# Optimization experiments

Measured on AMD Instinct MI355X. Metric: run time of the kernel, lower is better.

Reference implementation:

```python
import jax, jax.numpy as jnp
import numpy as np

B, S, D = 32, 1024, 1024   # batch, seq_len, d_model
P, F = 4, 4096             # num_phases, d_ff
# Each phase owns a contiguous split of S/P sequence positions (set_splits builds
# a disjoint contiguous partition of the sequence; assert t == seq_length).


def setup_inputs() -> dict:
    key = jax.random.key(0)
    ks = jax.random.split(key, 6)
    x = jax.random.normal(ks[0], (B, S, D), dtype=jnp.float32)
    phases = jax.random.randint(ks[1], (B, S), 0, P, dtype=jnp.int32)
    s1 = 1.0 / np.sqrt(D)
    s2 = 1.0 / np.sqrt(F)
    W1 = jax.random.uniform(ks[2], (P, D, F), jnp.float32, -s1, s1)
    b1 = jax.random.uniform(ks[3], (P, F), jnp.float32, -s1, s1)
    W2 = jax.random.uniform(ks[4], (P, F, D), jnp.float32, -s2, s2)
    b2 = jax.random.uniform(ks[5], (P, D), jnp.float32, -s2, s2)
    return {"x": x, "W1": W1, "b1": b1, "W2": W2, "b2": b2, "phases": phases}


def reference(x, W1, b1, W2, b2, phases):
    # Branched path (phases.ndim > 1): gather each phase's contiguous split,
    # run that phase's FF, scatter back. Since the static phase_mask is a
    # contiguous equal partition, gather/scatter == reshape into [B, P, S/P, D].
    xs = x.reshape(B, P, S // P, D)
    h = jax.nn.relu(jnp.einsum('bpsd,pdf->bpsf', xs, W1) + b1[None, :, None, :])
    y = jnp.einsum('bpsf,pfd->bpsd', h, W2) + b2[None, :, None, :]
    return y.reshape(B, S, D)
```

## Files before the change

### kernel.cpp

```cpp
#include <hip/hip_runtime.h>
#include <hip/hip_bf16.h>
#include <stdint.h>

typedef __bf16 bf16_t;
typedef bf16_t bf16x8 __attribute__((ext_vector_type(8)));
typedef bf16_t bf16x4 __attribute__((ext_vector_type(4)));
typedef float  f32x4  __attribute__((ext_vector_type(4)));

#define AS1(p) ((const __attribute__((address_space(1))) void*)(p))
#define AS3(p) ((__attribute__((address_space(3))) void*)(p))

static constexpr int B_ = 32, S_ = 1024, D_ = 1024, P_ = 4, F_ = 4096;
static constexpr int SPP = S_ / P_;
static constexpr int MP  = B_ * SPP;

__global__ void conv_x_kernel(const float* __restrict__ x, bf16_t* __restrict__ xg) {
  const int64_t n4 = (int64_t)B_ * S_ * D_ / 4;
  for (int64_t i = (int64_t)blockIdx.x * blockDim.x + threadIdx.x; i < n4;
       i += (int64_t)gridDim.x * blockDim.x) {
    int64_t e = i << 2;
    int d = (int)(e & (D_ - 1));
    int s = (int)((e >> 10) & (S_ - 1));
    int b = (int)(e >> 20);
    int p = s >> 8;
    int r = (b << 8) | (s & 255);
    const float4 v = ((const float4*)x)[i];
    bf16x4 o;
    o[0] = (bf16_t)v.x; o[1] = (bf16_t)v.y; o[2] = (bf16_t)v.z; o[3] = (bf16_t)v.w;
    *(bf16x4*)&xg[(((int64_t)p * MP + r) << 10) | d] = o;
  }
}

__global__ void conv_wt_kernel(const float* __restrict__ W, bf16_t* __restrict__ Wt,
                               int K, int N) {
  __shared__ bf16_t tile[32][33];
  const int p = blockIdx.z;
  const float* Wp = W + (int64_t)p * K * N;
  bf16_t* Wtp = Wt + (int64_t)p * K * N;
  const int n0 = blockIdx.x * 32, k0 = blockIdx.y * 32;
  const int tx = threadIdx.x & 31, ty = threadIdx.x >> 5;
  #pragma unroll
  for (int j = 0; j < 4; ++j) {
    int kr = ty + j * 8;
    tile[kr][tx] = (bf16_t)Wp[(int64_t)(k0 + kr) * N + n0 + tx];
  }
  __syncthreads();
  #pragma unroll
  for (int j = 0; j < 4; ++j) {
    int nr = ty + j * 8;
    Wtp[(int64_t)(n0 + nr) * K + k0 + tx] = tile[tx][nr];
  }
}


__device__ __forceinline__ bf16x8 ldsfrag(const char* region, int row, int cb) {
  return *(const bf16x8*)(region + row * 128 + (cb ^ ((row & 7) << 4)));
}

template<int LDK>
__device__ __forceinline__ void stage_half(const bf16_t* gsrc, char* ldsreg, int t) {
  #pragma unroll
  for (int j = 0; j < 2; ++j) {
    const int idx = j * 512 + t;
    const int row = idx >> 3;
    const int cb  = ((idx & 7) << 4) ^ ((row & 7) << 4);
    __builtin_amdgcn_global_load_lds(AS1((const char*)(gsrc + (int64_t)row * LDK) + cb),
                                     AS3(ldsreg + idx * 16), 16, 0, 0);
  }
}

#define MFMA_QUAD(AF, BF, MO, NO) \
  do { _Pragma("unroll") for (int m_ = 0; m_ < 4; ++m_) \
       _Pragma("unroll") for (int n_ = 0; n_ < 2; ++n_) \
       _Pragma("unroll") for (int k_ = 0; k_ < 2; ++k_) \
         acc[(MO) + m_][(NO) + n_] = __builtin_amdgcn_mfma_f32_16x16x32_bf16( \
             AF[m_][k_], BF[n_][k_], acc[(MO) + m_][(NO) + n_], 0, 0, 0); } while (0)

#define READ_A4(DST, REG, MO) \
  do { _Pragma("unroll") for (int m_ = 0; m_ < 4; ++m_) \
       _Pragma("unroll") for (int k_ = 0; k_ < 2; ++k_) \
         DST[m_][k_] = ldsfrag(REG, wm * 128 + ((MO) + m_) * 16 + fr, k_ * 64 + hi * 16); } while (0)

#define READ_B2(DST, REG, NO) \
  do { _Pragma("unroll") for (int n_ = 0; n_ < 2; ++n_) \
       _Pragma("unroll") for (int k_ = 0; k_ < 2; ++k_) \
         DST[n_][k_] = ldsfrag(REG, wn * 64 + ((NO) + n_) * 16 + fr, k_ * 64 + hi * 16); } while (0)

#define BAR()   __builtin_amdgcn_s_barrier()
#define SBAR()  __builtin_amdgcn_sched_barrier(0)
#define PRIO(x) __builtin_amdgcn_s_setprio(x)
#define VMCNT6() asm volatile("s_waitcnt vmcnt(6)" ::: "memory")
#define VMCNT0() asm volatile("s_waitcnt vmcnt(0)" ::: "memory")

template<bool RELU, bool OUT_BF16, int KK, int NN>
__global__ __launch_bounds__(512, 2)
void ffgemm8_kernel(const bf16_t* __restrict__ A, const bf16_t* __restrict__ Bt,
                    const float* __restrict__ bias, void* __restrict__ outv, int M) {
  static_assert(KK % 128 == 0, "need even number of 64-wide K tiles");
  __shared__ __align__(16) char smem[131072];
  char* const At0 = smem;
  char* const At1 = smem + 32768;
  char* const Bs0 = smem + 65536;
  char* const Bs1 = smem + 98304;

  const int t = threadIdx.x, lane = t & 63, w = t >> 6;
  const int wm = w >> 2, wn = w & 3;
  const int fr = lane & 15, hi = lane >> 4;

  const int gx = gridDim.x, gy = gridDim.y;
  const int nwg = gx * gy * (int)gridDim.z;
  const int id  = ((int)blockIdx.z * gy + (int)blockIdx.y) * gx + (int)blockIdx.x;
  const int swz = (id & 7) * (nwg >> 3) + (id >> 3);
  const int per_p = gx * gy;
  const int p  = swz / per_p;
  const int q  = swz % per_p;
  const int band = q / (gx * 4), qq = q % (gx * 4);
  const int bx = qq >> 2, by = band * 4 + (qq & 3);

  const int tile_m = by * 256, tile_n = bx * 256;
  const bf16_t* Ab = A  + (int64_t)p * M  * KK + (int64_t)tile_m * KK;
  const bf16_t* Bb = Bt + (int64_t)p * NN * KK + (int64_t)tile_n * KK;
  const float* biasp = bias + (int64_t)p * NN;

  f32x4 acc[8][4] = {};
  constexpr int NI = KK / 128;

  stage_half<KK>(Ab,                          At0,          t);
  stage_half<KK>(Ab + (int64_t)128 * KK,      At0 + 16384,  t);
  stage_half<KK>(Bb,                          Bs0,          t);
  stage_half<KK>(Bb + (int64_t)128 * KK,      Bs0 + 16384,  t);
  stage_half<KK>(Bb + 64,                     Bs1,          t);
  stage_half<KK>(Bb + (int64_t)128 * KK + 64, Bs1 + 16384,  t);
  stage_half<KK>(Ab + 64,                     At1,          t);
  VMCNT6();
  BAR(); SBAR();

  for (int i = 0; i < NI; ++i) {
    const int k0 = i * 128;
    const bool more = (i < NI - 1);
    bf16x8 a0[4][2], a1[4][2], b0[2][2], b1[2][2];

    READ_A4(a0, At0, 0); READ_B2(b0, Bs0, 0);
    PRIO(1); MFMA_QUAD(a0, b0, 0, 0); PRIO(0);
    READ_B2(b1, Bs0, 2);
    stage_half<KK>(Ab + (int64_t)128 * KK + (k0 + 64), At1 + 16384, t);
    SBAR(); BAR();
    PRIO(1); MFMA_QUAD(a0, b1, 0, 2); PRIO(0);
    READ_A4(a1, At0, 4);
    SBAR(); BAR();
    PRIO(1); MFMA_QUAD(a1, b0, 4, 0); PRIO(0);
    if (more) { stage_half<KK>(Bb + (k0 + 128), Bs0, t);
                stage_half<KK>(Bb + (int64_t)128 * KK + (k0 + 128), Bs0 + 16384, t); }
    SBAR(); BAR();
    PRIO(1); MFMA_QUAD(a1, b1, 4, 2); PRIO(0);
    if (more) stage_half<KK>(Ab + (k0 + 128), At0, t);
    if (more) VMCNT6(); else VMCNT0();
    SBAR(); BAR();

    READ_A4(a0, At1, 0); READ_B2(b0, Bs1, 0);
    PRIO(1); MFMA_QUAD(a0, b0, 0, 0); PRIO(0);
    READ_B2(b1, Bs1, 2);
    if (more) stage_half<KK>(Ab + (int64_t)128 * KK + (k0 + 128), At0 + 16384, t);
    SBAR(); BAR();
    PRIO(1); MFMA_QUAD(a0, b1, 0, 2); PRIO(0);
    READ_A4(a1, At1, 4);
    SBAR(); BAR();
    PRIO(1); MFMA_QUAD(a1, b0, 4, 0); PRIO(0);
    if (more) { stage_half<KK>(Bb + (k0 + 192), Bs1, t);
                stage_half<KK>(Bb + (int64_t)128 * KK + (k0 + 192), Bs1 + 16384, t); }
    SBAR(); BAR();
    PRIO(1); MFMA_QUAD(a1, b1, 4, 2); PRIO(0);
    if (more) stage_half<KK>(Ab + (k0 + 192), At1, t);
    if (more) VMCNT6(); else VMCNT0();
    SBAR(); BAR();
  }

  float bv[4];
  #pragma unroll
  for (int n = 0; n < 4; ++n) bv[n] = biasp[tile_n + wn * 64 + n * 16 + fr];
  if (OUT_BF16) {
    bf16_t* out = (bf16_t*)outv + (int64_t)p * M * NN;
    #pragma unroll
    for (int m = 0; m < 8; ++m)
      #pragma unroll
      for (int j = 0; j < 4; ++j) {
        const int row = tile_m + wm * 128 + m * 16 + hi * 4 + j;
        #pragma unroll
        for (int n = 0; n < 4; ++n) {
          const int col = tile_n + wn * 64 + n * 16 + fr;
          float v = acc[m][n][j] + bv[n];
          if (RELU) v = fmaxf(v, 0.0f);
          out[(int64_t)row * NN + col] = (bf16_t)v;
        }
      }
  } else {
    float* out = (float*)outv;
    #pragma unroll
    for (int m = 0; m < 8; ++m)
      #pragma unroll
      for (int j = 0; j < 4; ++j) {
        const int row = tile_m + wm * 128 + m * 16 + hi * 4 + j;
        const int grow = ((row >> 8) << 10) + p * SPP + (row & 255);
        #pragma unroll
        for (int n = 0; n < 4; ++n) {
          const int col = tile_n + wn * 64 + n * 16 + fr;
          out[(int64_t)grow * NN + col] = acc[m][n][j] + bv[n];
        }
      }
  }
}

extern "C" void kernel_launch(void* const* d_in, const int* in_sizes, int n_in,
                              void* d_out, int out_size, void* d_ws, size_t ws_size,
                              hipStream_t stream) {
  (void)in_sizes; (void)n_in; (void)out_size; (void)ws_size;
  const float* x  = (const float*)d_in[0];
  const float* W1 = (const float*)d_in[1];
  const float* b1 = (const float*)d_in[2];
  const float* W2 = (const float*)d_in[3];
  const float* b2 = (const float*)d_in[4];
  float* y = (float*)d_out;

  char* ws = (char*)d_ws;
  bf16_t* xg = (bf16_t*)ws;
  bf16_t* wt = (bf16_t*)(ws + (size_t)64 * 1024 * 1024);
  bf16_t* h  = (bf16_t*)(ws + (size_t)96 * 1024 * 1024);

  conv_x_kernel<<<2048, 256, 0, stream>>>(x, xg);
  conv_wt_kernel<<<dim3(F_ / 32, D_ / 32, P_), 256, 0, stream>>>(W1, wt, D_, F_);
  ffgemm8_kernel<true, true, 1024, 4096><<<dim3(F_ / 256, MP / 256, P_), 512, 0, stream>>>(
      xg, wt, b1, h, MP);
  conv_wt_kernel<<<dim3(D_ / 32, F_ / 32, P_), 256, 0, stream>>>(W2, wt, F_, D_);
  ffgemm8_kernel<false, false, 4096, 1024><<<dim3(D_ / 256, MP / 256, P_), 512, 0, stream>>>(
      h, wt, b2, y, MP);
}
```

Measured before the change: 552.6 us.

## Switch FF GEMM inner loop from 16x16x32 to 32x32x16 bf16 MFMA

Replaces the 16x16x32 MFMA tiling with 32x32x16 bf16 MFMA instructions. Each wave now holds a 4x2 grid of 32x32 accumulators and reads A/B fragments with a new lane mapping, issuing fewer LDS reads per FLOP. The epilogue row/column mapping is rewritten to match the 32x32 output layout. The goal is to cut LDS fragment-read traffic and instruction count. The cost is a different register schedule and more fragment registers held live (af[4][4]), which could pressure occupancy at launch_bounds(512,2).

```diff
diff --git a/kernel.cpp b/kernel.cpp
--- a/kernel.cpp
+++ b/kernel.cpp
@@ -5,7 +5,7 @@
 typedef __bf16 bf16_t;
 typedef bf16_t bf16x8 __attribute__((ext_vector_type(8)));
 typedef bf16_t bf16x4 __attribute__((ext_vector_type(4)));
-typedef float  f32x4  __attribute__((ext_vector_type(4)));
+typedef float  f32x16 __attribute__((ext_vector_type(16)));
 
 #define AS1(p) ((const __attribute__((address_space(1))) void*)(p))
 #define AS3(p) ((__attribute__((address_space(3))) void*)(p))
@@ -53,8 +53,8 @@
 }
 
 
-__device__ __forceinline__ bf16x8 ldsfrag(const char* region, int row, int cb) {
-  return *(const bf16x8*)(region + row * 128 + (cb ^ ((row & 7) << 4)));
+__device__ __forceinline__ bf16x8 ldsX(const char* region, int row, int kb) {
+  return *(const bf16x8*)(region + row * 128 + (kb ^ ((row & 7) << 4)));
 }
 
 template<int LDK>
@@ -69,22 +69,22 @@
   }
 }
 
-#define MFMA_QUAD(AF, BF, MO, NO) \
-  do { _Pragma("unroll") for (int m_ = 0; m_ < 4; ++m_) \
-       _Pragma("unroll") for (int n_ = 0; n_ < 2; ++n_) \
-       _Pragma("unroll") for (int k_ = 0; k_ < 2; ++k_) \
-         acc[(MO) + m_][(NO) + n_] = __builtin_amdgcn_mfma_f32_16x16x32_bf16( \
-             AF[m_][k_], BF[n_][k_], acc[(MO) + m_][(NO) + n_], 0, 0, 0); } while (0)
-
-#define READ_A4(DST, REG, MO) \
-  do { _Pragma("unroll") for (int m_ = 0; m_ < 4; ++m_) \
-       _Pragma("unroll") for (int k_ = 0; k_ < 2; ++k_) \
-         DST[m_][k_] = ldsfrag(REG, wm * 128 + ((MO) + m_) * 16 + fr, k_ * 64 + hi * 16); } while (0)
-
-#define READ_B2(DST, REG, NO) \
-  do { _Pragma("unroll") for (int n_ = 0; n_ < 2; ++n_) \
-       _Pragma("unroll") for (int k_ = 0; k_ < 2; ++k_) \
-         DST[n_][k_] = ldsfrag(REG, wn * 64 + ((NO) + n_) * 16 + fr, k_ * 64 + hi * 16); } while (0)
+#define MFMA32(A_, B_, C_) __builtin_amdgcn_mfma_f32_32x32x16_bf16(A_, B_, C_, 0, 0, 0)
+
+#define GRP(S0, MH0) \
+  do { _Pragma("unroll") for (int s_ = (S0); s_ < (S0) + 2; ++s_) \
+       _Pragma("unroll") for (int mh_ = (MH0); mh_ < (MH0) + 2; ++mh_) \
+       _Pragma("unroll") for (int nh_ = 0; nh_ < 2; ++nh_) \
+         acc[mh_][nh_] = MFMA32(af[mh_][s_], bf[nh_][s_], acc[mh_][nh_]); } while (0)
+
+#define RD_A(REG, MH, S0) \
+  do { _Pragma("unroll") for (int s_ = (S0); s_ < (S0) + 2; ++s_) \
+         af[MH][s_] = ldsX(REG, wm * 128 + (MH) * 32 + l31, s_ * 32 + hk16); } while (0)
+
+#define RD_B(REG, S0) \
+  do { _Pragma("unroll") for (int nh_ = 0; nh_ < 2; ++nh_) \
+       _Pragma("unroll") for (int s_ = (S0); s_ < (S0) + 2; ++s_) \
+         bf[nh_][s_] = ldsX(REG, wn * 64 + nh_ * 32 + l31, s_ * 32 + hk16); } while (0)
 
 #define BAR()   __builtin_amdgcn_s_barrier()
 #define SBAR()  __builtin_amdgcn_sched_barrier(0)
@@ -105,7 +105,7 @@
 
   const int t = threadIdx.x, lane = t & 63, w = t >> 6;
   const int wm = w >> 2, wn = w & 3;
-  const int fr = lane & 15, hi = lane >> 4;
+  const int l31 = lane & 31, hk = lane >> 5, hk16 = hk * 16;
 
   const int gx = gridDim.x, gy = gridDim.y;
   const int nwg = gx * gy * (int)gridDim.z;
@@ -122,7 +122,7 @@
   const bf16_t* Bb = Bt + (int64_t)p * NN * KK + (int64_t)tile_n * KK;
   const float* biasp = bias + (int64_t)p * NN;
 
-  f32x4 acc[8][4] = {};
+  f32x16 acc[4][2] = {};
   constexpr int NI = KK / 128;
 
   stage_half<KK>(Ab,                          At0,          t);
@@ -138,57 +138,59 @@
   for (int i = 0; i < NI; ++i) {
     const int k0 = i * 128;
     const bool more = (i < NI - 1);
-    bf16x8 a0[4][2], a1[4][2], b0[2][2], b1[2][2];
-
-    READ_A4(a0, At0, 0); READ_B2(b0, Bs0, 0);
-    PRIO(1); MFMA_QUAD(a0, b0, 0, 0); PRIO(0);
-    READ_B2(b1, Bs0, 2);
+    bf16x8 af[4][4], bf[2][4];
+
+    RD_A(At0, 0, 0); RD_A(At0, 1, 0); RD_B(Bs0, 0);
+    RD_A(At0, 0, 2); RD_A(At0, 1, 2);
+    PRIO(1); GRP(0, 0); PRIO(0);
     stage_half<KK>(Ab + (int64_t)128 * KK + (k0 + 64), At1 + 16384, t);
     SBAR(); BAR();
-    PRIO(1); MFMA_QUAD(a0, b1, 0, 2); PRIO(0);
-    READ_A4(a1, At0, 4);
-    SBAR(); BAR();
-    PRIO(1); MFMA_QUAD(a1, b0, 4, 0); PRIO(0);
+    RD_B(Bs0, 2);
+    PRIO(1); GRP(2, 0); PRIO(0);
+    SBAR(); BAR();
+    RD_A(At0, 2, 0); RD_A(At0, 3, 0); RD_A(At0, 2, 2); RD_A(At0, 3, 2);
+    PRIO(1); GRP(0, 2); PRIO(0);
     if (more) { stage_half<KK>(Bb + (k0 + 128), Bs0, t);
                 stage_half<KK>(Bb + (int64_t)128 * KK + (k0 + 128), Bs0 + 16384, t); }
     SBAR(); BAR();
-    PRIO(1); MFMA_QUAD(a1, b1, 4, 2); PRIO(0);
+    PRIO(1); GRP(2, 2); PRIO(0);
     if (more) stage_half<KK>(Ab + (k0 + 128), At0, t);
     if (more) VMCNT6(); else VMCNT0();
     SBAR(); BAR();
 
-    READ_A4(a0, At1, 0); READ_B2(b0, Bs1, 0);
-    PRIO(1); MFMA_QUAD(a0, b0, 0, 0); PRIO(0);
-    READ_B2(b1, Bs1, 2);
+    RD_A(At1, 0, 0); RD_A(At1, 1, 0); RD_B(Bs1, 0);
+    RD_A(At1, 0, 2); RD_A(At1, 1, 2);
+    PRIO(1); GRP(0, 0); PRIO(0);
     if (more) stage_half<KK>(Ab + (int64_t)128 * KK + (k0 + 128), At0 + 16384, t);
     SBAR(); BAR();
-    PRIO(1); MFMA_QUAD(a0, b1, 0, 2); PRIO(0);
-    READ_A4(a1, At1, 4);
-    SBAR(); BAR();
-    PRIO(1); MFMA_QUAD(a1, b0, 4, 0); PRIO(0);
+    RD_B(Bs1, 2);
+    PRIO(1); GRP(2, 0); PRIO(0);
+    SBAR(); BAR();
+    RD_A(At1, 2, 0); RD_A(At1, 3, 0); RD_A(At1, 2, 2); RD_A(At1, 3, 2);
+    PRIO(1); GRP(0, 2); PRIO(0);
     if (more) { stage_half<KK>(Bb + (k0 + 192), Bs1, t);
                 stage_half<KK>(Bb + (int64_t)128 * KK + (k0 + 192), Bs1 + 16384, t); }
     SBAR(); BAR();
-    PRIO(1); MFMA_QUAD(a1, b1, 4, 2); PRIO(0);
+    PRIO(1); GRP(2, 2); PRIO(0);
     if (more) stage_half<KK>(Ab + (k0 + 192), At1, t);
     if (more) VMCNT6(); else VMCNT0();
     SBAR(); BAR();
   }
 
-  float bv[4];
-  #pragma unroll
-  for (int n = 0; n < 4; ++n) bv[n] = biasp[tile_n + wn * 64 + n * 16 + fr];
+  float bv[2];
+  #pragma unroll
+  for (int nh = 0; nh < 2; ++nh) bv[nh] = biasp[tile_n + wn * 64 + nh * 32 + l31];
   if (OUT_BF16) {
     bf16_t* out = (bf16_t*)outv + (int64_t)p * M * NN;
     #pragma unroll
-    for (int m = 0; m < 8; ++m)
+    for (int mh = 0; mh < 4; ++mh)
       #pragma unroll
-      for (int j = 0; j < 4; ++j) {
-        const int row = tile_m + wm * 128 + m * 16 + hi * 4 + j;
+      for (int r = 0; r < 16; ++r) {
+        const int row = tile_m + wm * 128 + mh * 32 + (r & 3) + 8 * (r >> 2) + 4 * hk;
         #pragma unroll
-        for (int n = 0; n < 4; ++n) {
-          const int col = tile_n + wn * 64 + n * 16 + fr;
-          float v = acc[m][n][j] + bv[n];
+        for (int nh = 0; nh < 2; ++nh) {
+          const int col = tile_n + wn * 64 + nh * 32 + l31;
+          float v = acc[mh][nh][r] + bv[nh];
           if (RELU) v = fmaxf(v, 0.0f);
           out[(int64_t)row * NN + col] = (bf16_t)v;
         }
@@ -196,15 +198,15 @@
   } else {
     float* out = (float*)outv;
     #pragma unroll
-    for (int m = 0; m < 8; ++m)
+    for (int mh = 0; mh < 4; ++mh)
       #pragma unroll
-      for (int j = 0; j < 4; ++j) {
-        const int row = tile_m + wm * 128 + m * 16 + hi * 4 + j;
+      for (int r = 0; r < 16; ++r) {
+        const int row = tile_m + wm * 128 + mh * 32 + (r & 3) + 8 * (r >> 2) + 4 * hk;
         const int grow = ((row >> 8) << 10) + p * SPP + (row & 255);
         #pragma unroll
-        for (int n = 0; n < 4; ++n) {
-          const int col = tile_n + wn * 64 + n * 16 + fr;
-          out[(int64_t)grow * NN + col] = acc[m][n][j] + bv[n];
+        for (int nh = 0; nh < 2; ++nh) {
+          const int col = tile_n + wn * 64 + nh * 32 + l31;
+          out[(int64_t)grow * NN + col] = acc[mh][nh][r] + bv[nh];
         }
       }
   }
```

New measurement: 621.3 us. 1.12x slower.
